# Optimization experiments

Hardware: AMD Instinct MI355X
Metric: run time of the kernel (lower is better)

Reference implementation:

```python
import jax, jax.numpy as jnp
import numpy as np

EPS = 1e-8

def l2norm(x, axis=-1, eps=EPS):
    n = jnp.sqrt(jnp.sum(x * x, axis=axis, keepdims=True)) + eps
    return x / n

def setup_inputs() -> dict:
    key = jax.random.key(0)
    k1, k2, k3, k4 = jax.random.split(key, 4)
    B, Q, S, D, SIM = 512, 64, 36, 1024, 256
    query = jax.random.normal(k1, (B, Q, D), dtype=jnp.float32)
    context = jax.random.normal(k2, (B, S, D), dtype=jnp.float32)
    matrix = jax.random.uniform(k3, (B, Q, D), dtype=jnp.float32)
    W = jax.random.normal(k4, (SIM, D), dtype=jnp.float32) * 0.02
    b = jnp.zeros((SIM,), dtype=jnp.float32)
    return {"query": query, "context": context, "matrix": matrix,
            "W": W, "b": b, "smooth": 9}

def reference(query, context, matrix, W, b, smooth):
    # cross_attention
    q = query * matrix                                  # (B,Q,D)
    attn = jnp.einsum('bsd,bqd->bsq', context, q)       # (B,S,Q)
    attn = jnp.where(attn > 0, attn, 0.1 * attn)        # LeakyReLU(0.1)
    attn = l2norm(attn, axis=-1)                        # l2norm over Q
    attn = jnp.swapaxes(attn, 1, 2)                     # (B,Q,S)
    attn = jax.nn.softmax(attn * smooth, axis=2)        # temperature softmax over S
    wcontext = jnp.einsum('bqs,bsd->bqd', attn, context)
    wcontext = l2norm(wcontext, axis=-1)
    # Alignment_vector: squared diff -> linear -> l2norm
    sim_rep = (query - wcontext) ** 2                   # (B,Q,D)
    sim_rep = jnp.einsum('bqd,kd->bqk', sim_rep, W) + b # (B,Q,SIM)
    return l2norm(sim_rep, axis=-1)
```

## Files before the change

### kernel.cpp

```cpp
#include <hip/hip_runtime.h>
#include <hip/hip_bf16.h>

#define BB 512
#define QQ 64
#define SS 36
#define DD 1024
#define SIM 256

typedef unsigned short u16x8 __attribute__((ext_vector_type(8)));
typedef __bf16 bf16x8 __attribute__((ext_vector_type(8)));
typedef float f32x4 __attribute__((ext_vector_type(4)));
typedef unsigned short us;

__device__ __forceinline__ us f2bf(float f) {
  unsigned u = __float_as_uint(f);
  u += 0x7FFFu + ((u >> 16) & 1u);
  return (us)(u >> 16);
}
__device__ __forceinline__ float bf2f(us h) {
  return __uint_as_float(((unsigned)h) << 16);
}

__global__ __launch_bounds__(256) void k0_w16(const float* __restrict__ W,
                                              us* __restrict__ W16) {
  int i = blockIdx.x * 256 + threadIdx.x;
  float4 v = ((const float4*)W)[i];
  ushort4 p;
  p.x = f2bf(v.x); p.y = f2bf(v.y); p.z = f2bf(v.z); p.w = f2bf(v.w);
  ((ushort4*)W16)[i] = p;
}

#define KF_LDS 136192

template <bool USE_W16>
__global__ __launch_bounds__(512, 2) void k_fused(
    const float* __restrict__ query, const float* __restrict__ context,
    const float* __restrict__ matrix, const float* __restrict__ Wm,
    const float* __restrict__ bvec, const int* __restrict__ smoothp,
    const us* __restrict__ W16, float* __restrict__ out) {
  extern __shared__ __align__(16) char smem[];
  us* ctxL = (us*)smem;
  us* qmL = (us*)(smem + 99072);
  float* sc = (float*)(smem + 99072);
  us* A16s = (us*)(smem + 99072);
  us* P16s = (us*)(smem + 116480);
  us* Gf16L = (us*)(smem + 125696);
  float* biasL = (float*)(smem + 132608);
  float* rnL = (float*)(smem + 133632);
  float* rsum = (float*)(smem + 133888);

  const int t = threadIdx.x, bb = blockIdx.x;
  const int lane = t & 63, w = t >> 6;
  const int ml = lane & 15, kg = lane >> 4;
  const float smf = (float)smoothp[0];

  for (int idx = t; idx < 6192; idx += 512)
    ((unsigned*)(ctxL + 36 * 1032))[idx] = 0;
  for (int idx = t; idx < 2304; idx += 512) ((unsigned*)P16s)[idx] = 0;
  for (int idx = t; idx < 1728; idx += 512) ((unsigned*)Gf16L)[idx] = 0;
  if (t < 256) biasL[t] = bvec[t];

  u16x8 qr0[8], qr1[8];

  f32x4 acc[3], gacc[3];
#pragma unroll
  for (int j = 0; j < 3; ++j) {
    acc[j] = (f32x4){0.f, 0.f, 0.f, 0.f};
    gacc[j] = (f32x4){0.f, 0.f, 0.f, 0.f};
  }

#pragma unroll
  for (int ch = 0; ch < 8; ++ch) {
    const int d0 = ch * 128;
#pragma unroll
    for (int i = 0; i < 2; ++i) {
      int idx = t + 512 * i;
      int row = idx >> 4, c8 = idx & 15;
      const float4* gq = (const float4*)&query[((size_t)bb * QQ + row) * DD + d0 + c8 * 8];
      const float4* gm = (const float4*)&matrix[((size_t)bb * QQ + row) * DD + d0 + c8 * 8];
      float4 a0 = gq[0], a1 = gq[1], m0 = gm[0], m1 = gm[1];
      u16x8 pk;
      pk[0] = f2bf(a0.x * m0.x); pk[1] = f2bf(a0.y * m0.y);
      pk[2] = f2bf(a0.z * m0.z); pk[3] = f2bf(a0.w * m0.w);
      pk[4] = f2bf(a1.x * m1.x); pk[5] = f2bf(a1.y * m1.y);
      pk[6] = f2bf(a1.z * m1.z); pk[7] = f2bf(a1.w * m1.w);
      *(u16x8*)&qmL[row * 136 + c8 * 8] = pk;
    }
    {
      int row = t >> 4, c8 = t & 15;
      const float4* gc = (const float4*)&context[((size_t)bb * SS + row) * DD + d0 + c8 * 8];
      float4 a0 = gc[0], a1 = gc[1];
      u16x8 pk;
      pk[0] = f2bf(a0.x); pk[1] = f2bf(a0.y); pk[2] = f2bf(a0.z); pk[3] = f2bf(a0.w);
      pk[4] = f2bf(a1.x); pk[5] = f2bf(a1.y); pk[6] = f2bf(a1.z); pk[7] = f2bf(a1.w);
      *(u16x8*)&ctxL[row * 1032 + d0 + c8 * 8] = pk;
    }
    if (t < 64) {
      int row = 32 + (t >> 4), c8 = t & 15;
      const float4* gc = (const float4*)&context[((size_t)bb * SS + row) * DD + d0 + c8 * 8];
      float4 a0 = gc[0], a1 = gc[1];
      u16x8 pk;
      pk[0] = f2bf(a0.x); pk[1] = f2bf(a0.y); pk[2] = f2bf(a0.z); pk[3] = f2bf(a0.w);
      pk[4] = f2bf(a1.x); pk[5] = f2bf(a1.y); pk[6] = f2bf(a1.z); pk[7] = f2bf(a1.w);
      *(u16x8*)&ctxL[row * 1032 + d0 + c8 * 8] = pk;
    }
    float sv[16];
    {
      const float* qcol = query + (size_t)bb * QQ * DD + d0 + w * 16 + ml;
#pragma unroll
      for (int j = 0; j < 16; ++j) {
        int q = (j >> 2) * 16 + kg * 4 + (j & 3);
        sv[j] = qcol[(size_t)q * DD];
      }
    }
    __syncthreads();
#pragma unroll
    for (int ks = 0; ks < 4; ++ks) {
      const int ko = ks * 32 + kg * 8;
      if (w < 4) {
        bf16x8 bq = __builtin_bit_cast(bf16x8, *(const u16x8*)&qmL[(w * 16 + ml) * 136 + ko]);
#pragma unroll
        for (int mt = 0; mt < 3; ++mt) {
          bf16x8 af = __builtin_bit_cast(
              bf16x8, *(const u16x8*)&ctxL[(mt * 16 + ml) * 1032 + d0 + ko]);
          acc[mt] = __builtin_amdgcn_mfma_f32_16x16x32_bf16(af, bq, acc[mt], 0, 0, 0);
        }
      } else if (w < 7) {
        bf16x8 ai = __builtin_bit_cast(
            bf16x8, *(const u16x8*)&ctxL[((w - 4) * 16 + ml) * 1032 + d0 + ko]);
#pragma unroll
        for (int j = 0; j < 3; ++j) {
          bf16x8 aj = __builtin_bit_cast(
              bf16x8, *(const u16x8*)&ctxL[(j * 16 + ml) * 1032 + d0 + ko]);
          gacc[j] = __builtin_amdgcn_mfma_f32_16x16x32_bf16(ai, aj, gacc[j], 0, 0, 0);
        }
      }
    }
    {
      u16x8 s0, s1;
#pragma unroll
      for (int j = 0; j < 8; ++j) {
        s0[j] = f2bf(sv[j]);
        s1[j] = f2bf(sv[8 + j]);
      }
      qr0[ch] = s0;
      qr1[ch] = s1;
    }
    __syncthreads();
  }

  if (w < 4) {
#pragma unroll
    for (int mt = 0; mt < 3; ++mt)
#pragma unroll
      for (int ii = 0; ii < 4; ++ii) {
        float v = acc[mt][ii];
        v = v > 0.f ? v : 0.1f * v;
        sc[(mt * 16 + kg * 4 + ii) * 68 + w * 16 + ml] = v;
      }
  } else if (w < 7) {
#pragma unroll
    for (int j = 0; j < 3; ++j)
#pragma unroll
      for (int ii = 0; ii < 4; ++ii)
        Gf16L[((w - 4) * 16 + kg * 4 + ii) * 72 + j * 16 + ml] = f2bf(gacc[j][ii]);
  }
  __syncthreads();

  if (t < 36) {
    float ssum = 0.f;
    for (int qi = 0; qi < 64; ++qi) { float v = sc[t * 68 + qi]; ssum = fmaf(v, v, ssum); }
    float rn = 1.f / (sqrtf(ssum) + 1e-8f);
    for (int qi = 0; qi < 64; ++qi) sc[t * 68 + qi] *= rn;
  }
  __syncthreads();

  if (t < 64) {
    float mx = -1e30f;
    for (int s2 = 0; s2 < 36; ++s2) mx = fmaxf(mx, sc[s2 * 68 + t]);
    float sum = 0.f;
    float ev[36];
    for (int s2 = 0; s2 < 36; ++s2) {
      float e = __expf((sc[s2 * 68 + t] - mx) * smf);
      ev[s2] = e;
      sum += e;
    }
    float rs = 1.f / sum;
#pragma unroll
    for (int s2 = 0; s2 < 36; ++s2) P16s[t * 72 + s2] = f2bf(ev[s2] * rs);
  }
  __syncthreads();

  if (w < 3) {
    f32x4 accv[4];
#pragma unroll
    for (int mt = 0; mt < 4; ++mt) accv[mt] = (f32x4){0.f, 0.f, 0.f, 0.f};
#pragma unroll
    for (int ks = 0; ks < 2; ++ks) {
      const int ko = ks * 32 + kg * 8;
      bf16x8 gfr = __builtin_bit_cast(bf16x8, *(const u16x8*)&Gf16L[(w * 16 + ml) * 72 + ko]);
#pragma unroll
      for (int mt = 0; mt < 4; ++mt) {
        bf16x8 pf = __builtin_bit_cast(bf16x8, *(const u16x8*)&P16s[(mt * 16 + ml) * 72 + ko]);
        accv[mt] = __builtin_amdgcn_mfma_f32_16x16x32_bf16(pf, gfr, accv[mt], 0, 0, 0);
      }
    }
#pragma unroll
    for (int mt = 0; mt < 4; ++mt)
#pragma unroll
      for (int ii = 0; ii < 4; ++ii) {
        int q = mt * 16 + kg * 4 + ii;
        float vv = accv[mt][ii] * bf2f(P16s[q * 72 + w * 16 + ml]);
        vv += __shfl_xor(vv, 1);
        vv += __shfl_xor(vv, 2);
        vv += __shfl_xor(vv, 4);
        vv += __shfl_xor(vv, 8);
        if (ml == 0) rsum[q * 4 + w] = vv;
      }
  }
  __syncthreads();
  if (t < 64) {
    float s2 = rsum[t * 4] + rsum[t * 4 + 1] + rsum[t * 4 + 2];
    rnL[t] = 1.f / (sqrtf(s2) + 1e-8f);
  }
  __syncthreads();

  f32x4 accs[4][2];
#pragma unroll
  for (int mt = 0; mt < 4; ++mt)
#pragma unroll
    for (int ntl = 0; ntl < 2; ++ntl) accs[mt][ntl] = (f32x4){0.f, 0.f, 0.f, 0.f};

#pragma unroll
  for (int ch = 0; ch < 8; ++ch) {
    const int d0 = ch * 128;
    f32x4 aw[4];
#pragma unroll
    for (int mt = 0; mt < 4; ++mt) aw[mt] = (f32x4){0.f, 0.f, 0.f, 0.f};
    {
      const int ncol = d0 + w * 16 + ml;
      u16x8 g0;
#pragma unroll
      for (int j = 0; j < 8; ++j) g0[j] = ctxL[(kg * 8 + j) * 1032 + ncol];
      bf16x8 bfr0 = __builtin_bit_cast(bf16x8, g0);
#pragma unroll
      for (int mt = 0; mt < 4; ++mt) {
        bf16x8 af = __builtin_bit_cast(bf16x8, *(const u16x8*)&P16s[(mt * 16 + ml) * 72 + kg * 8]);
        aw[mt] = __builtin_amdgcn_mfma_f32_16x16x32_bf16(af, bfr0, aw[mt], 0, 0, 0);
      }
      u16x8 g1;
#pragma unroll
      for (int j = 0; j < 8; ++j)
        g1[j] = (kg < 2) ? ctxL[(32 + kg * 8 + j) * 1032 + ncol] : (us)0;
      bf16x8 bfr1 = __builtin_bit_cast(bf16x8, g1);
#pragma unroll
      for (int mt = 0; mt < 4; ++mt) {
        bf16x8 af =
            __builtin_bit_cast(bf16x8, *(const u16x8*)&P16s[(mt * 16 + ml) * 72 + 32 + kg * 8]);
        aw[mt] = __builtin_amdgcn_mfma_f32_16x16x32_bf16(af, bfr1, aw[mt], 0, 0, 0);
      }
    }
    __syncthreads();
#pragma unroll
    for (int mt = 0; mt < 4; ++mt)
#pragma unroll
      for (int ii = 0; ii < 4; ++ii) {
        int q = mt * 16 + kg * 4 + ii;
        const int e = mt * 4 + ii;
        float qv = bf2f(e < 8 ? qr0[ch][e] : qr1[ch][e - 8]);
        float av = qv - aw[mt][ii] * rnL[q];
        A16s[q * 136 + w * 16 + ml] = f2bf(av * av);
      }
    __syncthreads();
#pragma unroll
    for (int ks = 0; ks < 4; ++ks) {
      const int ko = ks * 32 + kg * 8;
      bf16x8 bfr[2];
#pragma unroll
      for (int ntl = 0; ntl < 2; ++ntl) {
        const size_t wrow = (size_t)(w * 32 + ntl * 16 + ml);
        if constexpr (USE_W16) {
          bfr[ntl] = __builtin_bit_cast(bf16x8, *(const u16x8*)&W16[wrow * DD + d0 + ko]);
        } else {
          const float4* wp = (const float4*)&Wm[wrow * DD + d0 + ko];
          float4 x = wp[0], y = wp[1];
          u16x8 pk;
          pk[0] = f2bf(x.x); pk[1] = f2bf(x.y); pk[2] = f2bf(x.z); pk[3] = f2bf(x.w);
          pk[4] = f2bf(y.x); pk[5] = f2bf(y.y); pk[6] = f2bf(y.z); pk[7] = f2bf(y.w);
          bfr[ntl] = __builtin_bit_cast(bf16x8, pk);
        }
      }
#pragma unroll
      for (int mt = 0; mt < 4; ++mt) {
        bf16x8 af = __builtin_bit_cast(bf16x8, *(const u16x8*)&A16s[(mt * 16 + ml) * 136 + ko]);
#pragma unroll
        for (int ntl = 0; ntl < 2; ++ntl)
          accs[mt][ntl] =
              __builtin_amdgcn_mfma_f32_16x16x32_bf16(af, bfr[ntl], accs[mt][ntl], 0, 0, 0);
      }
    }
  }
  __syncthreads();

#pragma unroll
  for (int mt = 0; mt < 4; ++mt)
#pragma unroll
    for (int ii = 0; ii < 4; ++ii) {
      int q = mt * 16 + kg * 4 + ii;
      float partial = 0.f;
#pragma unroll
      for (int ntl = 0; ntl < 2; ++ntl) {
        int col = w * 32 + ntl * 16 + ml;
        float v = accs[mt][ntl][ii] + biasL[col];
        partial = fmaf(v, v, partial);
      }
      partial += __shfl_xor(partial, 1);
      partial += __shfl_xor(partial, 2);
      partial += __shfl_xor(partial, 4);
      partial += __shfl_xor(partial, 8);
      if (ml == 0) rsum[q * 9 + w] = partial;
    }
  __syncthreads();
  if (t < 64) {
    float ssum = 0.f;
#pragma unroll
    for (int w2 = 0; w2 < 8; ++w2) ssum += rsum[t * 9 + w2];
    rnL[t] = 1.f / (sqrtf(ssum) + 1e-8f);
  }
  __syncthreads();
#pragma unroll
  for (int mt = 0; mt < 4; ++mt)
#pragma unroll
    for (int ntl = 0; ntl < 2; ++ntl)
#pragma unroll
      for (int ii = 0; ii < 4; ++ii) {
        int q = mt * 16 + kg * 4 + ii;
        int col = w * 32 + ntl * 16 + ml;
        float v = accs[mt][ntl][ii] + biasL[col];
        out[((size_t)bb * QQ + q) * SIM + col] = v * rnL[q];
      }
}

extern "C" void kernel_launch(void* const* d_in, const int* in_sizes, int n_in,
                              void* d_out, int out_size, void* d_ws, size_t ws_size,
                              hipStream_t stream) {
  const float* query = (const float*)d_in[0];
  const float* context = (const float*)d_in[1];
  const float* matrix = (const float*)d_in[2];
  const float* Wm = (const float*)d_in[3];
  const float* bvec = (const float*)d_in[4];
  const int* smoothp = (const int*)d_in[5];
  float* out = (float*)d_out;

  us* W16 = (us*)d_ws;
  const bool useW16 = ws_size >= (size_t)SIM * DD * 2;

  hipFuncSetAttribute((const void*)k_fused<true>,
                      hipFuncAttributeMaxDynamicSharedMemorySize, KF_LDS);
  hipFuncSetAttribute((const void*)k_fused<false>,
                      hipFuncAttributeMaxDynamicSharedMemorySize, KF_LDS);

  if (useW16) {
    k0_w16<<<dim3(SIM * DD / 1024), dim3(256), 0, stream>>>(Wm, W16);
    k_fused<true><<<dim3(BB), dim3(512), KF_LDS, stream>>>(query, context, matrix, Wm,
                                                           bvec, smoothp, W16, out);
  } else {
    k_fused<false><<<dim3(BB), dim3(512), KF_LDS, stream>>>(query, context, matrix, Wm,
                                                            bvec, smoothp, W16, out);
  }
}
```

Baseline: 142.5 us.

## Double the block to 1024 threads and software-pipeline global loads

Doubles the workgroup to 16 waves so each wave owns one 16x16 MFMA tile instead of three or two, spreading the score, Gram and final projection GEMMs across more waves. The query*matrix and context chunk loads for the next 128-wide slice are issued before the current slice's MFMAs, using double-buffered qm LDS tiles, so only one barrier is needed per chunk. LDS use grows to about 152KB, which means only one block fits per CU, so the extra waves per block replace the previous two-block residency. Waves 8-15 sit idle in the qr/aw stages.

```diff
diff --git a/kernel.cpp b/kernel.cpp
--- a/kernel.cpp
+++ b/kernel.cpp
@@ -30,113 +30,125 @@
   ((ushort4*)W16)[i] = p;
 }
 
-#define KF_LDS 136192
+#define KF_LDS 155648
 
 template <bool USE_W16>
-__global__ __launch_bounds__(512, 2) void k_fused(
+__global__ __launch_bounds__(1024, 4) void k_fused(
     const float* __restrict__ query, const float* __restrict__ context,
     const float* __restrict__ matrix, const float* __restrict__ Wm,
     const float* __restrict__ bvec, const int* __restrict__ smoothp,
     const us* __restrict__ W16, float* __restrict__ out) {
   extern __shared__ __align__(16) char smem[];
   us* ctxL = (us*)smem;
-  us* qmL = (us*)(smem + 99072);
+  us* qmA = (us*)(smem + 99072);
+  us* qmB = (us*)(smem + 116480);
   float* sc = (float*)(smem + 99072);
   us* A16s = (us*)(smem + 99072);
-  us* P16s = (us*)(smem + 116480);
-  us* Gf16L = (us*)(smem + 125696);
-  float* biasL = (float*)(smem + 132608);
-  float* rnL = (float*)(smem + 133632);
-  float* rsum = (float*)(smem + 133888);
+  us* P16s = (us*)(smem + 133888);
+  us* Gf16L = (us*)(smem + 143104);
+  float* biasL = (float*)(smem + 150016);
+  float* rnL = (float*)(smem + 151040);
+  float* rsum = (float*)(smem + 151296);
 
   const int t = threadIdx.x, bb = blockIdx.x;
   const int lane = t & 63, w = t >> 6;
   const int ml = lane & 15, kg = lane >> 4;
   const float smf = (float)smoothp[0];
 
-  for (int idx = t; idx < 6192; idx += 512)
+  for (int idx = t; idx < 6192; idx += 1024)
     ((unsigned*)(ctxL + 36 * 1032))[idx] = 0;
-  for (int idx = t; idx < 2304; idx += 512) ((unsigned*)P16s)[idx] = 0;
-  for (int idx = t; idx < 1728; idx += 512) ((unsigned*)Gf16L)[idx] = 0;
+  for (int idx = t; idx < 2304; idx += 1024) ((unsigned*)P16s)[idx] = 0;
+  for (int idx = t; idx < 1728; idx += 1024) ((unsigned*)Gf16L)[idx] = 0;
   if (t < 256) biasL[t] = bvec[t];
 
+  const int srow = t >> 4, sc8 = t & 15;
+  const float* qrow = query + ((size_t)bb * QQ + srow) * DD + sc8 * 8;
+  const float* mrow = matrix + ((size_t)bb * QQ + srow) * DD + sc8 * 8;
+  const float* crow = context + ((size_t)bb * SS + (srow < 36 ? srow : 0)) * DD + sc8 * 8;
+  const float* qcol = query + (size_t)bb * QQ * DD + w * 16 + ml;
+
   u16x8 qr0[8], qr1[8];
 
-  f32x4 acc[3], gacc[3];
-#pragma unroll
-  for (int j = 0; j < 3; ++j) {
-    acc[j] = (f32x4){0.f, 0.f, 0.f, 0.f};
-    gacc[j] = (f32x4){0.f, 0.f, 0.f, 0.f};
-  }
+  f32x4 acc[3];
+#pragma unroll
+  for (int j = 0; j < 3; ++j) acc[j] = (f32x4){0.f, 0.f, 0.f, 0.f};
+
+  {
+    float4 a0 = *(const float4*)(qrow + 0), a1 = *(const float4*)(qrow + 4);
+    float4 m0 = *(const float4*)(mrow + 0), m1 = *(const float4*)(mrow + 4);
+    u16x8 pk;
+    pk[0] = f2bf(a0.x * m0.x); pk[1] = f2bf(a0.y * m0.y);
+    pk[2] = f2bf(a0.z * m0.z); pk[3] = f2bf(a0.w * m0.w);
+    pk[4] = f2bf(a1.x * m1.x); pk[5] = f2bf(a1.y * m1.y);
+    pk[6] = f2bf(a1.z * m1.z); pk[7] = f2bf(a1.w * m1.w);
+    *(u16x8*)&qmA[srow * 136 + sc8 * 8] = pk;
+    if (t < 576) {
+      float4 c0 = *(const float4*)(crow + 0), c1 = *(const float4*)(crow + 4);
+      u16x8 ck;
+      ck[0] = f2bf(c0.x); ck[1] = f2bf(c0.y); ck[2] = f2bf(c0.z); ck[3] = f2bf(c0.w);
+      ck[4] = f2bf(c1.x); ck[5] = f2bf(c1.y); ck[6] = f2bf(c1.z); ck[7] = f2bf(c1.w);
+      *(u16x8*)&ctxL[srow * 1032 + sc8 * 8] = ck;
+    }
+  }
+  __syncthreads();
 
 #pragma unroll
   for (int ch = 0; ch < 8; ++ch) {
-    const int d0 = ch * 128;
-#pragma unroll
-    for (int i = 0; i < 2; ++i) {
-      int idx = t + 512 * i;
-      int row = idx >> 4, c8 = idx & 15;
-      const float4* gq = (const float4*)&query[((size_t)bb * QQ + row) * DD + d0 + c8 * 8];
-      const float4* gm = (const float4*)&matrix[((size_t)bb * QQ + row) * DD + d0 + c8 * 8];
-      float4 a0 = gq[0], a1 = gq[1], m0 = gm[0], m1 = gm[1];
+    const int d0 = ch * 128, dn = d0 + 128;
+    float4 a0, a1, m0, m1, c0, c1;
+    if (ch < 7) {
+      a0 = *(const float4*)(qrow + dn); a1 = *(const float4*)(qrow + dn + 4);
+      m0 = *(const float4*)(mrow + dn); m1 = *(const float4*)(mrow + dn + 4);
+      if (t < 576) {
+        c0 = *(const float4*)(crow + dn); c1 = *(const float4*)(crow + dn + 4);
+      }
+    }
+    float sv[16];
+    if (w < 8) {
+#pragma unroll
+      for (int j = 0; j < 16; ++j) {
+        int q = (j >> 2) * 16 + kg * 4 + (j & 3);
+        sv[j] = qcol[(size_t)q * DD + d0];
+      }
+    }
+    __builtin_amdgcn_sched_barrier(0);
+    const us* qmCur = (ch & 1) ? qmB : qmA;
+#pragma unroll
+    for (int ks = 0; ks < 4; ++ks) {
+      const int ko = ks * 32 + kg * 8;
+      if (w < 12) {
+        const int mt = w >> 2, nt = w & 3;
+        bf16x8 bq = __builtin_bit_cast(bf16x8, *(const u16x8*)&qmCur[(nt * 16 + ml) * 136 + ko]);
+        bf16x8 af = __builtin_bit_cast(
+            bf16x8, *(const u16x8*)&ctxL[(mt * 16 + ml) * 1032 + d0 + ko]);
+        acc[0] = __builtin_amdgcn_mfma_f32_16x16x32_bf16(af, bq, acc[0], 0, 0, 0);
+      } else if (w < 15) {
+        bf16x8 ai = __builtin_bit_cast(
+            bf16x8, *(const u16x8*)&ctxL[((w - 12) * 16 + ml) * 1032 + d0 + ko]);
+#pragma unroll
+        for (int j = 0; j < 3; ++j) {
+          bf16x8 aj = __builtin_bit_cast(
+              bf16x8, *(const u16x8*)&ctxL[(j * 16 + ml) * 1032 + d0 + ko]);
+          acc[j] = __builtin_amdgcn_mfma_f32_16x16x32_bf16(ai, aj, acc[j], 0, 0, 0);
+        }
+      }
+    }
+    if (ch < 7) {
+      us* qdst = ((ch + 1) & 1) ? qmB : qmA;
       u16x8 pk;
       pk[0] = f2bf(a0.x * m0.x); pk[1] = f2bf(a0.y * m0.y);
       pk[2] = f2bf(a0.z * m0.z); pk[3] = f2bf(a0.w * m0.w);
       pk[4] = f2bf(a1.x * m1.x); pk[5] = f2bf(a1.y * m1.y);
       pk[6] = f2bf(a1.z * m1.z); pk[7] = f2bf(a1.w * m1.w);
-      *(u16x8*)&qmL[row * 136 + c8 * 8] = pk;
-    }
-    {
-      int row = t >> 4, c8 = t & 15;
-      const float4* gc = (const float4*)&context[((size_t)bb * SS + row) * DD + d0 + c8 * 8];
-      float4 a0 = gc[0], a1 = gc[1];
-      u16x8 pk;
-      pk[0] = f2bf(a0.x); pk[1] = f2bf(a0.y); pk[2] = f2bf(a0.z); pk[3] = f2bf(a0.w);
-      pk[4] = f2bf(a1.x); pk[5] = f2bf(a1.y); pk[6] = f2bf(a1.z); pk[7] = f2bf(a1.w);
-      *(u16x8*)&ctxL[row * 1032 + d0 + c8 * 8] = pk;
-    }
-    if (t < 64) {
-      int row = 32 + (t >> 4), c8 = t & 15;
-      const float4* gc = (const float4*)&context[((size_t)bb * SS + row) * DD + d0 + c8 * 8];
-      float4 a0 = gc[0], a1 = gc[1];
-      u16x8 pk;
-      pk[0] = f2bf(a0.x); pk[1] = f2bf(a0.y); pk[2] = f2bf(a0.z); pk[3] = f2bf(a0.w);
-      pk[4] = f2bf(a1.x); pk[5] = f2bf(a1.y); pk[6] = f2bf(a1.z); pk[7] = f2bf(a1.w);
-      *(u16x8*)&ctxL[row * 1032 + d0 + c8 * 8] = pk;
-    }
-    float sv[16];
-    {
-      const float* qcol = query + (size_t)bb * QQ * DD + d0 + w * 16 + ml;
-#pragma unroll
-      for (int j = 0; j < 16; ++j) {
-        int q = (j >> 2) * 16 + kg * 4 + (j & 3);
-        sv[j] = qcol[(size_t)q * DD];
-      }
-    }
-    __syncthreads();
-#pragma unroll
-    for (int ks = 0; ks < 4; ++ks) {
-      const int ko = ks * 32 + kg * 8;
-      if (w < 4) {
-        bf16x8 bq = __builtin_bit_cast(bf16x8, *(const u16x8*)&qmL[(w * 16 + ml) * 136 + ko]);
-#pragma unroll
-        for (int mt = 0; mt < 3; ++mt) {
-          bf16x8 af = __builtin_bit_cast(
-              bf16x8, *(const u16x8*)&ctxL[(mt * 16 + ml) * 1032 + d0 + ko]);
-          acc[mt] = __builtin_amdgcn_mfma_f32_16x16x32_bf16(af, bq, acc[mt], 0, 0, 0);
-        }
-      } else if (w < 7) {
-        bf16x8 ai = __builtin_bit_cast(
-            bf16x8, *(const u16x8*)&ctxL[((w - 4) * 16 + ml) * 1032 + d0 + ko]);
-#pragma unroll
-        for (int j = 0; j < 3; ++j) {
-          bf16x8 aj = __builtin_bit_cast(
-              bf16x8, *(const u16x8*)&ctxL[(j * 16 + ml) * 1032 + d0 + ko]);
-          gacc[j] = __builtin_amdgcn_mfma_f32_16x16x32_bf16(ai, aj, gacc[j], 0, 0, 0);
-        }
-      }
-    }
-    {
+      *(u16x8*)&qdst[srow * 136 + sc8 * 8] = pk;
+      if (t < 576) {
+        u16x8 ck;
+        ck[0] = f2bf(c0.x); ck[1] = f2bf(c0.y); ck[2] = f2bf(c0.z); ck[3] = f2bf(c0.w);
+        ck[4] = f2bf(c1.x); ck[5] = f2bf(c1.y); ck[6] = f2bf(c1.z); ck[7] = f2bf(c1.w);
+        *(u16x8*)&ctxL[srow * 1032 + dn + sc8 * 8] = ck;
+      }
+    }
+    if (w < 8) {
       u16x8 s0, s1;
 #pragma unroll
       for (int j = 0; j < 8; ++j) {
@@ -149,21 +161,20 @@
     __syncthreads();
   }
 
-  if (w < 4) {
-#pragma unroll
-    for (int mt = 0; mt < 3; ++mt)
-#pragma unroll
-      for (int ii = 0; ii < 4; ++ii) {
-        float v = acc[mt][ii];
-        v = v > 0.f ? v : 0.1f * v;
-        sc[(mt * 16 + kg * 4 + ii) * 68 + w * 16 + ml] = v;
-      }
-  } else if (w < 7) {
+  if (w < 12) {
+    const int mt = w >> 2, nt = w & 3;
+#pragma unroll
+    for (int ii = 0; ii < 4; ++ii) {
+      float v = acc[0][ii];
+      v = v > 0.f ? v : 0.1f * v;
+      sc[(mt * 16 + kg * 4 + ii) * 68 + nt * 16 + ml] = v;
+    }
+  } else if (w < 15) {
 #pragma unroll
     for (int j = 0; j < 3; ++j)
 #pragma unroll
       for (int ii = 0; ii < 4; ++ii)
-        Gf16L[((w - 4) * 16 + kg * 4 + ii) * 72 + j * 16 + ml] = f2bf(gacc[j][ii]);
+        Gf16L[((w - 12) * 16 + kg * 4 + ii) * 72 + j * 16 + ml] = f2bf(acc[j][ii]);
   }
   __syncthreads();
 
@@ -225,11 +236,9 @@
   }
   __syncthreads();
 
-  f32x4 accs[4][2];
-#pragma unroll
-  for (int mt = 0; mt < 4; ++mt)
-#pragma unroll
-    for (int ntl = 0; ntl < 2; ++ntl) accs[mt][ntl] = (f32x4){0.f, 0.f, 0.f, 0.f};
+  f32x4 accs[4];
+#pragma unroll
+  for (int mt = 0; mt < 4; ++mt) accs[mt] = (f32x4){0.f, 0.f, 0.f, 0.f};
 
 #pragma unroll
   for (int ch = 0; ch < 8; ++ch) {
@@ -237,7 +246,7 @@
     f32x4 aw[4];
 #pragma unroll
     for (int mt = 0; mt < 4; ++mt) aw[mt] = (f32x4){0.f, 0.f, 0.f, 0.f};
-    {
+    if (w < 8) {
       const int ncol = d0 + w * 16 + ml;
       u16x8 g0;
 #pragma unroll
@@ -261,42 +270,38 @@
       }
     }
     __syncthreads();
-#pragma unroll
-    for (int mt = 0; mt < 4; ++mt)
-#pragma unroll
-      for (int ii = 0; ii < 4; ++ii) {
-        int q = mt * 16 + kg * 4 + ii;
-        const int e = mt * 4 + ii;
-        float qv = bf2f(e < 8 ? qr0[ch][e] : qr1[ch][e - 8]);
-        float av = qv - aw[mt][ii] * rnL[q];
-        A16s[q * 136 + w * 16 + ml] = f2bf(av * av);
-      }
+    if (w < 8) {
+#pragma unroll
+      for (int mt = 0; mt < 4; ++mt)
+#pragma unroll
+        for (int ii = 0; ii < 4; ++ii) {
+          int q = mt * 16 + kg * 4 + ii;
+          const int e = mt * 4 + ii;
+          float qv = bf2f(e < 8 ? qr0[ch][e] : qr1[ch][e - 8]);
+          float av = qv - aw[mt][ii] * rnL[q];
+          A16s[q * 136 + w * 16 + ml] = f2bf(av * av);
+        }
+    }
     __syncthreads();
 #pragma unroll
     for (int ks = 0; ks < 4; ++ks) {
       const int ko = ks * 32 + kg * 8;
-      bf16x8 bfr[2];
-#pragma unroll
-      for (int ntl = 0; ntl < 2; ++ntl) {
-        const size_t wrow = (size_t)(w * 32 + ntl * 16 + ml);
-        if constexpr (USE_W16) {
-          bfr[ntl] = __builtin_bit_cast(bf16x8, *(const u16x8*)&W16[wrow * DD + d0 + ko]);
-        } else {
-          const float4* wp = (const float4*)&Wm[wrow * DD + d0 + ko];
-          float4 x = wp[0], y = wp[1];
-          u16x8 pk;
-          pk[0] = f2bf(x.x); pk[1] = f2bf(x.y); pk[2] = f2bf(x.z); pk[3] = f2bf(x.w);
-          pk[4] = f2bf(y.x); pk[5] = f2bf(y.y); pk[6] = f2bf(y.z); pk[7] = f2bf(y.w);
-          bfr[ntl] = __builtin_bit_cast(bf16x8, pk);
-        }
+      bf16x8 bfr;
+      if constexpr (USE_W16) {
+        bfr = __builtin_bit_cast(
+            bf16x8, *(const u16x8*)&W16[(size_t)(w * 16 + ml) * DD + d0 + ko]);
+      } else {
+        const float4* wp = (const float4*)&Wm[(size_t)(w * 16 + ml) * DD + d0 + ko];
+        float4 x = wp[0], y = wp[1];
+        u16x8 pk;
+        pk[0] = f2bf(x.x); pk[1] = f2bf(x.y); pk[2] = f2bf(x.z); pk[3] = f2bf(x.w);
+        pk[4] = f2bf(y.x); pk[5] = f2bf(y.y); pk[6] = f2bf(y.z); pk[7] = f2bf(y.w);
+        bfr = __builtin_bit_cast(bf16x8, pk);
       }
 #pragma unroll
       for (int mt = 0; mt < 4; ++mt) {
         bf16x8 af = __builtin_bit_cast(bf16x8, *(const u16x8*)&A16s[(mt * 16 + ml) * 136 + ko]);
-#pragma unroll
-        for (int ntl = 0; ntl < 2; ++ntl)
-          accs[mt][ntl] =
-              __builtin_amdgcn_mfma_f32_16x16x32_bf16(af, bfr[ntl], accs[mt][ntl], 0, 0, 0);
+        accs[mt] = __builtin_amdgcn_mfma_f32_16x16x32_bf16(af, bfr, accs[mt], 0, 0, 0);
       }
     }
   }
@@ -307,38 +312,31 @@
 #pragma unroll
     for (int ii = 0; ii < 4; ++ii) {
       int q = mt * 16 + kg * 4 + ii;
-      float partial = 0.f;
-#pragma unroll
-      for (int ntl = 0; ntl < 2; ++ntl) {
-        int col = w * 32 + ntl * 16 + ml;
-        float v = accs[mt][ntl][ii] + biasL[col];
-        partial = fmaf(v, v, partial);
-      }
+      float v = accs[mt][ii] + biasL[w * 16 + ml];
+      float partial = v * v;
       partial += __shfl_xor(partial, 1);
       partial += __shfl_xor(partial, 2);
       partial += __shfl_xor(partial, 4);
       partial += __shfl_xor(partial, 8);
-      if (ml == 0) rsum[q * 9 + w] = partial;
+      if (ml == 0) rsum[q * 17 + w] = partial;
     }
   __syncthreads();
   if (t < 64) {
     float ssum = 0.f;
 #pragma unroll
-    for (int w2 = 0; w2 < 8; ++w2) ssum += rsum[t * 9 + w2];
+    for (int w2 = 0; w2 < 16; ++w2) ssum += rsum[t * 17 + w2];
     rnL[t] = 1.f / (sqrtf(ssum) + 1e-8f);
   }
   __syncthreads();
 #pragma unroll
   for (int mt = 0; mt < 4; ++mt)
 #pragma unroll
-    for (int ntl = 0; ntl < 2; ++ntl)
-#pragma unroll
-      for (int ii = 0; ii < 4; ++ii) {
-        int q = mt * 16 + kg * 4 + ii;
-        int col = w * 32 + ntl * 16 + ml;
-        float v = accs[mt][ntl][ii] + biasL[col];
-        out[((size_t)bb * QQ + q) * SIM + col] = v * rnL[q];
-      }
+    for (int ii = 0; ii < 4; ++ii) {
+      int q = mt * 16 + kg * 4 + ii;
+      int col = w * 16 + ml;
+      float v = accs[mt][ii] + biasL[col];
+      out[((size_t)bb * QQ + q) * SIM + col] = v * rnL[q];
+    }
 }
 
 extern "C" void kernel_launch(void* const* d_in, const int* in_sizes, int n_in,
@@ -362,10 +360,10 @@
 
   if (useW16) {
     k0_w16<<<dim3(SIM * DD / 1024), dim3(256), 0, stream>>>(Wm, W16);
-    k_fused<true><<<dim3(BB), dim3(512), KF_LDS, stream>>>(query, context, matrix, Wm,
-                                                           bvec, smoothp, W16, out);
+    k_fused<true><<<dim3(BB), dim3(1024), KF_LDS, stream>>>(query, context, matrix, Wm,
+                                                            bvec, smoothp, W16, out);
   } else {
-    k_fused<false><<<dim3(BB), dim3(512), KF_LDS, stream>>>(query, context, matrix, Wm,
-                                                            bvec, smoothp, W16, out);
-  }
-}
+    k_fused<false><<<dim3(BB), dim3(1024), KF_LDS, stream>>>(query, context, matrix, Wm,
+                                                             bvec, smoothp, W16, out);
+  }
+}
```

Result: slower. 154.6 us (+8.5%).
